# Kernel tuning notes

Hardware: AMD Instinct MI355X
Metric: run time of the kernel (lower is better)

Reference implementation:

```python
import jax, jax.numpy as jnp
import numpy as np

N_BATCH, CH, HW, KERNEL, STRIDE, VC = 8, 256, 96, 8, 3, 512


def setup_inputs() -> dict:
    key = jax.random.key(0)
    k0, k1, k2, k3 = jax.random.split(key, 4)
    kk = KERNEL * KERNEL
    x = jax.random.normal(k0, (N_BATCH, CH, HW, HW), dtype=jnp.float32)
    # 1x1 conv weight [vc, ch, 1, 1] stored as [vc, ch]
    conv_w = jax.random.normal(k1, (VC, CH), dtype=jnp.float32) * 0.05
    # integrate_mask_activation: Linear(ch+kk, 3ch) -> LeakyReLU(0.2) -> Linear(3ch, ch) -> Tanh
    W1 = jax.random.normal(k2, (3 * CH, CH + kk), dtype=jnp.float32) * 0.02
    b1 = jnp.zeros((3 * CH,), dtype=jnp.float32)
    W2 = jax.random.normal(k3, (CH, 3 * CH), dtype=jnp.float32) * 0.02
    b2 = jnp.zeros((CH,), dtype=jnp.float32)
    return {"x": x, "conv_w": conv_w, "W1": W1, "b1": b1, "W2": W2, "b2": b2}


def _unfold(x, k, s):
    # torch.nn.Unfold(kernel=(k,k), stride=s) -> patches [n, L, c, k, k]
    n, c, h, w = x.shape
    oh = (h - k) // s + 1
    ow = (w - k) // s + 1
    ih = (jnp.arange(oh) * s)[:, None] + jnp.arange(k)[None, :]  # [oh, k]
    iw = (jnp.arange(ow) * s)[:, None] + jnp.arange(k)[None, :]  # [ow, k]
    p = x[:, :, ih, :]          # [n, c, oh, k, w]
    p = p[:, :, :, :, iw]       # [n, c, oh, k, ow, k]
    p = p.transpose(0, 2, 4, 1, 3, 5)  # [n, oh, ow, c, k, k]
    return p.reshape(n, oh * ow, c, k, k), oh * ow


def reference(x, conv_w, W1, b1, W2, b2):
    k = KERNEL
    kk = k * k
    n, c, h, w = x.shape
    patches, L = _unfold(x, k, STRIDE)           # [n, L, c, k, k]
    N = n * L
    p = patches.reshape(N, c, k, k)

    # GenerateMask_2_0: normalized similarity via 1x1 conv
    x_norm = jnp.sqrt((p ** 2).sum(1))           # [N, k, k]
    w_norm = jnp.sqrt((conv_w ** 2).sum(1))      # [vc]
    y = jnp.einsum('nchw,vc->nvhw', p, conv_w)   # [N, vc, k, k]
    y = y / (x_norm[:, None, :, :] * w_norm[None, :, None, None])

    vc = conv_w.shape[0]
    y_flat = y.reshape(N, vc * kk)
    idx = jnp.argmax(y_flat, axis=1)                       # topk(k=1)
    max_sim = jnp.take_along_axis(y_flat, idx[:, None], axis=1)  # [N, 1]
    max_ch = idx // kk                                     # codebook index [N]
    col = idx % kk                                         # spatial index [N]

    rows = jnp.arange(N)
    sim_map_max = y.reshape(N, vc, kk)[rows, max_ch]       # [N, kk]
    max_act = p.reshape(N, c, kk)[rows, :, col]            # [N, c]
    vc_vec = conv_w[max_ch]                                # [N, c]
    integ = max_act * max_sim + vc_vec * (1.0 - max_sim)   # blend with codebook

    # integrate_mask_activation MLP
    inp = jnp.concatenate([integ, sim_map_max], axis=1)    # [N, c + kk]
    h1 = inp @ W1.T + b1
    h1 = jnp.where(h1 > 0, h1, 0.2 * h1)                   # LeakyReLU(0.2)
    out = jnp.tanh(h1 @ W2.T + b2)                         # [N, c]
    return out.reshape(n, L, c)
```

## Files before the change

kernel.cpp:

```cpp
#include <hip/hip_runtime.h>
#include <hip/hip_fp16.h>
#include <math.h>

#define NB 8
#define CHN 256
#define HWD 96
#define PIXN (HWD*HWD)
#define TOTPIX (NB*PIXN)
#define VCN 512
#define OHW 30
#define LPP (OHW*OHW)
#define NPATCH (NB*LPP)
#define INPD 320
#define HID 768
#define MTP 456

typedef unsigned short u16;
typedef __attribute__((ext_vector_type(8))) short bf16x8;
typedef __attribute__((ext_vector_type(8))) unsigned short us8;
typedef __attribute__((ext_vector_type(4))) float f32x4;

__device__ __forceinline__ float f4c(const float4 v, int i){
  return i==0 ? v.x : i==1 ? v.y : i==2 ? v.z : v.w;
}
__device__ __forceinline__ u16 bfrn(float f){
  unsigned u = __float_as_uint(f);
  return (u16)((u + 0x7fffu + ((u>>16)&1u)) >> 16);
}
__device__ __forceinline__ float bf2f(u16 h){
  return __uint_as_float(((unsigned)h)<<16);
}


template<int NS>
__device__ __forceinline__ void split_body(const float* __restrict__ src,
                                           u16* __restrict__ dst, int K,
                                           int rt, int kk, int kkc, int lane){
  const int qr = lane>>4, col = lane&15;
  const float* s = src + (size_t)(rt*16+col)*K + kk*32 + qr*8;
  us8 h1, h2, h3;
  #pragma unroll
  for (int j=0;j<8;j++){
    float a = s[j];
    u16 x1 = bfrn(a);  float r1 = a - bf2f(x1);
    u16 x2 = bfrn(r1); float r2 = r1 - bf2f(x2);
    h1[j]=x1; h2[j]=x2; h3[j]=bfrn(r2);
  }
  size_t base = ((size_t)(rt*kkc + kk)*NS)*512 + lane*8;
  *(us8*)&dst[base]     = h1;
  *(us8*)&dst[base+512] = h2;
  if (NS == 3) *(us8*)&dst[base+1024] = h3;
}

__global__ __launch_bounds__(64) void prep_k(
    const float* __restrict__ cw, const float* __restrict__ W1,
    const float* __restrict__ W2, u16* __restrict__ wf,
    u16* __restrict__ w1f, u16* __restrict__ w2f, float* __restrict__ invw){
  int b = blockIdx.x;
  const int lane = threadIdx.x;
  if (b < 256){ split_body<3>(cw, wf, CHN, b>>3, b&7, 8, lane); return; }
  b -= 256;
  if (b < 480){ split_body<2>(W1, w1f, INPD, b/10, b%10, 10, lane); return; }
  b -= 480;
  if (b < 384){ split_body<2>(W2, w2f, HID, b/24, b%24, 24, lane); return; }
  b -= 384;
  const float4 a = *(const float4*)&cw[(size_t)b*CHN + lane*4];
  float s = fmaf(a.x,a.x, fmaf(a.y,a.y, fmaf(a.z,a.z, a.w*a.w)));
  #pragma unroll
  for (int off=32; off; off>>=1) s += __shfl_xor(s, off);
  if (lane==0) invw[b] = 1.0f/sqrtf(s);
}

__device__ __forceinline__ void mfma6(f32x4& c, const bf16x8* A, const bf16x8* B){
  c = __builtin_amdgcn_mfma_f32_16x16x32_bf16(A[0], B[0], c, 0,0,0);
  c = __builtin_amdgcn_mfma_f32_16x16x32_bf16(A[0], B[1], c, 0,0,0);
  c = __builtin_amdgcn_mfma_f32_16x16x32_bf16(A[1], B[0], c, 0,0,0);
  c = __builtin_amdgcn_mfma_f32_16x16x32_bf16(A[0], B[2], c, 0,0,0);
  c = __builtin_amdgcn_mfma_f32_16x16x32_bf16(A[1], B[1], c, 0,0,0);
  c = __builtin_amdgcn_mfma_f32_16x16x32_bf16(A[2], B[0], c, 0,0,0);
}

__global__ __launch_bounds__(256,3) void gemm_z_k(
    const float* __restrict__ x, const u16* __restrict__ wf,
    const float* __restrict__ invw,
    float* __restrict__ pbest, int* __restrict__ pbidx,
    __half* __restrict__ zf){
  __shared__ __align__(16) u16 afr[2*8*3*512];
  __shared__ float ssq2[4][32];
  __shared__ float rv[32][4];
  __shared__ int   ri[32][4];
  const int t = threadIdx.x;
  const int wv = t>>6, lane = t&63;
  const int col = lane&15, qr = lane>>4;
  const size_t p0 = (size_t)blockIdx.x * 32;
  const int img = (int)(p0 / PIXN);
  const int pl0 = (int)(p0 % PIXN);

  {
    const int pi = t & 31, bq = t >> 5;
    const int fr = pi & 15, mt = pi >> 4;
    const float* xb = x + ((size_t)img*CHN)*PIXN + pl0 + pi;
    float s = 0.f;
    #pragma unroll
    for (int it=0; it<4; ++it){
      const int c0 = it*64 + bq*8;
      float xv[8];
      #pragma unroll
      for (int j=0;j<8;j++) xv[j] = xb[(size_t)(c0+j)*PIXN];
      us8 h1,h2,h3;
      #pragma unroll
      for (int j=0;j<8;j++){
        const float a = xv[j];
        s = fmaf(a,a,s);
        u16 x1 = bfrn(a);  float r1 = a - bf2f(x1);
        u16 x2 = bfrn(r1);
        h1[j]=x1; h2[j]=x2; h3[j]=bfrn(r1 - bf2f(x2));
      }
      const int kk = c0 >> 5, cq = (c0>>3)&3;
      u16* dstp = &afr[((mt*8+kk)*3)*512 + (cq*16+fr)*8];
      *(us8*)dstp        = h1;
      *(us8*)(dstp+512)  = h2;
      *(us8*)(dstp+1024) = h3;
    }
    s += __shfl_xor(s, 32);
    if (lane < 32) ssq2[wv][lane] = s;
  }
  __syncthreads();

  f32x4 acc[2][8];
  #pragma unroll
  for (int i=0;i<2;i++)
    #pragma unroll
    for (int j=0;j<8;j++) acc[i][j] = (f32x4){0.f,0.f,0.f,0.f};
  const size_t loff = (size_t)lane*8;
  const int loff16 = lane*8;
  for (int kk=0; kk<8; ++kk){
    bf16x8 a0[3], a1[3];
    {
      const int ab0 = (kk*3)*512 + loff16;
      const int ab1 = ((8+kk)*3)*512 + loff16;
      a0[0] = *(const bf16x8*)&afr[ab0];
      a0[1] = *(const bf16x8*)&afr[ab0+512];
      a0[2] = *(const bf16x8*)&afr[ab0+1024];
      a1[0] = *(const bf16x8*)&afr[ab1];
      a1[1] = *(const bf16x8*)&afr[ab1+512];
      a1[2] = *(const bf16x8*)&afr[ab1+1024];
    }
    #pragma unroll
    for (int h=0; h<2; ++h){
      bf16x8 bg[4][3];
      #pragma unroll
      for (int q=0;q<4;q++){
        const int ni = h*4+q;
        const size_t bb = (((size_t)(wv*8+ni)*8 + kk)*3)*512 + loff;
        bg[q][0] = *(const bf16x8*)&wf[bb];
        bg[q][1] = *(const bf16x8*)&wf[bb+512];
        bg[q][2] = *(const bf16x8*)&wf[bb+1024];
      }
      #pragma unroll
      for (int q=0;q<4;q++){
        const int ni = h*4+q;
        mfma6(acc[0][ni], a0, bg[q]);
        mfma6(acc[1][ni], a1, bg[q]);
      }
    }
  }

  float iw[8];
  #pragma unroll
  for (int ni=0;ni<8;ni++) iw[ni] = invw[wv*128 + ni*16 + col];
  #pragma unroll
  for (int mi=0;mi<2;mi++){
    #pragma unroll
    for (int r=0;r<4;r++){
      const int P2 = mi*16 + qr*4 + r;
      const float sq = ssq2[0][P2] + ssq2[1][P2] + ssq2[2][P2] + ssq2[3][P2];
      const float ip = rsqrtf(sq);
      float bz = -1e30f; int bvi = 0;
      #pragma unroll
      for (int ni=0;ni<8;ni++){
        const float z = f4c(*(const float4*)&acc[mi][ni], r) * ip * iw[ni];
        const int vv = wv*128 + ni*16 + col;
        zf[(p0+P2)*VCN + vv] = __float2half(z);
        if (z > bz){ bz = z; bvi = vv; }
      }
      #pragma unroll
      for (int off=1; off<16; off<<=1){
        const float oz = __shfl_xor(bz, off);
        const int  oi = __shfl_xor(bvi, off);
        if (oz > bz || (oz == bz && oi < bvi)){ bz = oz; bvi = oi; }
      }
      if (col == 0){ rv[P2][wv] = bz; ri[P2][wv] = bvi; }
    }
  }
  __syncthreads();
  if (t < 32){
    float best = rv[t][0]; int bi = ri[t][0];
    #pragma unroll
    for (int s=1;s<4;s++){
      float z2 = rv[t][s]; int i2 = ri[t][s];
      if (z2 > best || (z2 == best && i2 < bi)){ best = z2; bi = i2; }
    }
    pbest[p0+t] = best; pbidx[p0+t] = bi;
  }
}

__global__ __launch_bounds__(64) void select_k(
    const float* __restrict__ x, const float* __restrict__ cw,
    const __half* __restrict__ zf,
    const float* __restrict__ pbest, const int* __restrict__ pbidx,
    u16* __restrict__ inpf){
  __shared__ float wlds[256];
  __shared__ float xcol[256];
  __shared__ float simv[64];
  const int q = blockIdx.x;
  const int lane = threadIdx.x;
  const int n = q / LPP, l = q % LPP;
  const int oy = l / OHW, ox = l % OHW;
  const int pl = (oy*3 + (lane >> 3))*HWD + (ox*3 + (lane & 7));
  const int p = n*PIXN + pl;
  const int rt = q >> 4, ql = q & 15;
  float val = pbest[p];
  int flat = pbidx[p]*64 + lane;
  #pragma unroll
  for (int off=32; off>0; off>>=1){
    float ov = __shfl_xor(val, off);
    int of = __shfl_xor(flat, off);
    if (ov > val || (ov == val && of < flat)){ val = ov; flat = of; }
  }
  const int mch = flat >> 6;
  const int pos = flat & 63;
  const float ms = val;
  *(float4*)&wlds[lane*4] = *(const float4*)&cw[(size_t)mch*CHN + lane*4];
  simv[lane] = __half2float(zf[(size_t)p*VCN + mch]);
  const int wpl = (oy*3 + (pos>>3))*HWD + (ox*3 + (pos&7));
  const float* xb = x + (size_t)n*CHN*PIXN + wpl;
  #pragma unroll
  for (int j=0;j<4;j++) xcol[lane*4+j] = xb[(size_t)(lane*4+j)*PIXN];
  __syncthreads();
  if (lane < 32){
    const int kk = lane >> 2, qr = lane & 3;
    const float om = 1.0f - ms;
    const int c0 = kk*32 + qr*8;
    us8 p1, p2;
    #pragma unroll
    for (int j=0;j<8;j++){
      float v = fmaf(xcol[c0+j], ms, wlds[c0+j]*om);
      u16 s1 = bfrn(v);
      p1[j] = s1; p2[j] = bfrn(v - bf2f(s1));
    }
    const size_t ob = ((size_t)(rt*10 + kk)*2)*512 + (qr*16 + ql)*8;
    *(us8*)&inpf[ob]     = p1;
    *(us8*)&inpf[ob+512] = p2;
  }
  if (lane < 16){
    const int s = lane >> 3, kk = 8 + ((lane >> 2) & 1), qr = lane & 3;
    us8 pv;
    #pragma unroll
    for (int j=0;j<8;j++){
      float v = simv[(kk-8)*32 + qr*8 + j];
      u16 s1 = bfrn(v);
      pv[j] = (s == 0) ? s1 : bfrn(v - bf2f(s1));
    }
    const size_t ob = ((size_t)(rt*10 + kk)*2 + s)*512 + (qr*16 + ql)*8;
    *(us8*)&inpf[ob] = pv;
  }
}

__global__ __launch_bounds__(256,2) void mlp1_k(
    const u16* __restrict__ af, const u16* __restrict__ bf,
    const float* __restrict__ bias, u16* __restrict__ h1f){
  const int kkc = INPD >> 5;
  const int t = threadIdx.x;
  const int n0 = blockIdx.x*128, m0 = blockIdx.y*128;
  const int lane = t&63, wv = t>>6;
  const int mq = wv&1, nq = wv>>1;
  const int col = lane&15, qr = lane>>4;
  const size_t loff = (size_t)lane*8;
  const int ptA0 = (m0>>4) + mq*4;
  const int ntB0 = (n0>>4) + nq*4;
  f32x4 acc[4][4];
  #pragma unroll
  for (int i=0;i<4;i++)
    #pragma unroll
    for (int j=0;j<4;j++) acc[i][j] = (f32x4){0.f,0.f,0.f,0.f};

  for (int kk=0; kk<kkc; kk++){
    bf16x8 a[4][2];
    #pragma unroll
    for (int mi=0;mi<4;mi++){
      const size_t ab = (((size_t)(ptA0+mi)*kkc + kk)*2)*512 + loff;
      a[mi][0] = *(const bf16x8*)&af[ab];
      a[mi][1] = *(const bf16x8*)&af[ab+512];
    }
    #pragma unroll
    for (int ni=0;ni<4;ni++){
      const size_t bb = (((size_t)(ntB0+ni)*kkc + kk)*2)*512 + loff;
      const bf16x8 b1 = *(const bf16x8*)&bf[bb];
      const bf16x8 b2 = *(const bf16x8*)&bf[bb+512];
      #pragma unroll
      for (int mi=0;mi<4;mi++){
        f32x4 c = acc[mi][ni];
        c = __builtin_amdgcn_mfma_f32_16x16x32_bf16(a[mi][0], b1, c, 0,0,0);
        c = __builtin_amdgcn_mfma_f32_16x16x32_bf16(a[mi][0], b2, c, 0,0,0);
        c = __builtin_amdgcn_mfma_f32_16x16x32_bf16(a[mi][1], b1, c, 0,0,0);
        acc[mi][ni] = c;
      }
    }
  }
  float bb4[4];
  #pragma unroll
  for (int ni=0;ni<4;ni++) bb4[ni] = bias[n0 + nq*64 + ni*16 + col];
  #pragma unroll
  for (int mi=0;mi<4;mi++){
    const int rt2 = (m0>>4) + mq*4 + mi;
    #pragma unroll
    for (int r=0;r<4;r++){
      #pragma unroll
      for (int ni=0;ni<4;ni++){
        float v = f4c(*(const float4*)&acc[mi][ni], r) + bb4[ni];
        v = v > 0.f ? v : 0.2f*v;
        u16 s1 = bfrn(v);
        u16 s2 = bfrn(v - bf2f(s1));
        const int kk2 = (n0>>5) + nq*2 + (ni>>1);
        const int qn = (ni&1)*2 + (col>>3);
        const size_t ob = ((size_t)(rt2*24 + kk2)*2)*512 + (qn*16 + qr*4 + r)*8 + (col&7);
        h1f[ob] = s1; h1f[ob+512] = s2;
      }
    }
  }
}

__global__ __launch_bounds__(256,2) void mlp2_k(
    const u16* __restrict__ af, const u16* __restrict__ bf,
    const float* __restrict__ bias, float* __restrict__ C){
  const int kkc = HID >> 5;
  const int t = threadIdx.x;
  const int n0 = blockIdx.x*128, m0 = blockIdx.y*128;
  const int lane = t&63, wv = t>>6;
  const int mq = wv&1, nq = wv>>1;
  const int col = lane&15, qr = lane>>4;
  const size_t loff = (size_t)lane*8;
  const int ptA0 = (m0>>4) + mq*4;
  const int ntB0 = (n0>>4) + nq*4;
  f32x4 acc[4][4];
  #pragma unroll
  for (int i=0;i<4;i++)
    #pragma unroll
    for (int j=0;j<4;j++) acc[i][j] = (f32x4){0.f,0.f,0.f,0.f};

  for (int kk=0; kk<kkc; kk++){
    bf16x8 a[4][2];
    #pragma unroll
    for (int mi=0;mi<4;mi++){
      const size_t ab = (((size_t)(ptA0+mi)*kkc + kk)*2)*512 + loff;
      a[mi][0] = *(const bf16x8*)&af[ab];
      a[mi][1] = *(const bf16x8*)&af[ab+512];
    }
    #pragma unroll
    for (int ni=0;ni<4;ni++){
      const size_t bb = (((size_t)(ntB0+ni)*kkc + kk)*2)*512 + loff;
      const bf16x8 b1 = *(const bf16x8*)&bf[bb];
      const bf16x8 b2 = *(const bf16x8*)&bf[bb+512];
      #pragma unroll
      for (int mi=0;mi<4;mi++){
        f32x4 c = acc[mi][ni];
        c = __builtin_amdgcn_mfma_f32_16x16x32_bf16(a[mi][0], b1, c, 0,0,0);
        c = __builtin_amdgcn_mfma_f32_16x16x32_bf16(a[mi][0], b2, c, 0,0,0);
        c = __builtin_amdgcn_mfma_f32_16x16x32_bf16(a[mi][1], b1, c, 0,0,0);
        acc[mi][ni] = c;
      }
    }
  }
  float bb4[4];
  #pragma unroll
  for (int ni=0;ni<4;ni++) bb4[ni] = bias[n0 + nq*64 + ni*16 + col];
  #pragma unroll
  for (int mi=0;mi<4;mi++){
    #pragma unroll
    for (int r=0;r<4;r++){
      const int row = m0 + mq*64 + mi*16 + qr*4 + r;
      if (row < NPATCH){
        #pragma unroll
        for (int ni=0;ni<4;ni++){
          float v = f4c(*(const float4*)&acc[mi][ni], r) + bb4[ni];
          C[(size_t)row*CHN + n0 + nq*64 + ni*16 + col] = tanhf(v);
        }
      }
    }
  }
}

extern "C" void kernel_launch(void* const* d_in, const int* in_sizes, int n_in,
                              void* d_out, int out_size, void* d_ws, size_t ws_size,
                              hipStream_t stream){
  const float* x  = (const float*)d_in[0];
  const float* cw = (const float*)d_in[1];
  const float* W1 = (const float*)d_in[2];
  const float* b1 = (const float*)d_in[3];
  const float* W2 = (const float*)d_in[4];
  const float* b2 = (const float*)d_in[5];
  float* out = (float*)d_out;
  float* ws = (float*)d_ws;
  float* invw  = ws;
  float* pbest = invw + VCN;
  int*   pbidx = (int*)(pbest + TOTPIX);
  u16*   wf    = (u16*)(pbidx + TOTPIX);
  u16*   w1f   = wf + (size_t)32*8*3*512;
  u16*   w2f   = w1f + (size_t)48*10*2*512;
  u16*   inpf  = w2f + (size_t)16*24*2*512;
  __half* zf   = (__half*)(inpf + (size_t)MTP*10*2*512);
  u16*   h1f   = (u16*)zf;

  prep_k<<<1632,64,0,stream>>>(cw, W1, W2, wf, w1f, w2f, invw);
  gemm_z_k<<<TOTPIX/32,256,0,stream>>>(x, wf, invw, pbest, pbidx, zf);
  select_k<<<NPATCH,64,0,stream>>>(x, cw, zf, pbest, pbidx, inpf);
  mlp1_k<<<dim3(HID/128, (NPATCH+127)/128),256,0,stream>>>(inpf, w1f, b1, h1f);
  mlp2_k<<<dim3(CHN/128, (NPATCH+127)/128),256,0,stream>>>(h1f, w2f, b2, out);
}
```

Before: 326.4 us.

## Fuse all stages into one persistent kernel with grid-wide barriers

Replaces the five separate launches (weight prep, similarity GEMM, patch selection, two MLP GEMMs) with one persistent kernel. Its grid is sized from the occupancy query and it loops over the work units of each stage, separated by atomic-counter grid barriers. The aim is to remove launch gaps and tail effects between stages. In exchange it uses spin barriers that depend on every block being co-resident, and the MLP stages now run at a different occupancy than their original launch bounds. The old multi-kernel path remains as a fallback.

```diff
diff --git a/kernel.cpp b/kernel.cpp
--- a/kernel.cpp
+++ b/kernel.cpp
@@ -52,25 +52,6 @@
   if (NS == 3) *(us8*)&dst[base+1024] = h3;
 }
 
-__global__ __launch_bounds__(64) void prep_k(
-    const float* __restrict__ cw, const float* __restrict__ W1,
-    const float* __restrict__ W2, u16* __restrict__ wf,
-    u16* __restrict__ w1f, u16* __restrict__ w2f, float* __restrict__ invw){
-  int b = blockIdx.x;
-  const int lane = threadIdx.x;
-  if (b < 256){ split_body<3>(cw, wf, CHN, b>>3, b&7, 8, lane); return; }
-  b -= 256;
-  if (b < 480){ split_body<2>(W1, w1f, INPD, b/10, b%10, 10, lane); return; }
-  b -= 480;
-  if (b < 384){ split_body<2>(W2, w2f, HID, b/24, b%24, 24, lane); return; }
-  b -= 384;
-  const float4 a = *(const float4*)&cw[(size_t)b*CHN + lane*4];
-  float s = fmaf(a.x,a.x, fmaf(a.y,a.y, fmaf(a.z,a.z, a.w*a.w)));
-  #pragma unroll
-  for (int off=32; off; off>>=1) s += __shfl_xor(s, off);
-  if (lane==0) invw[b] = 1.0f/sqrtf(s);
-}
-
 __device__ __forceinline__ void mfma6(f32x4& c, const bf16x8* A, const bf16x8* B){
   c = __builtin_amdgcn_mfma_f32_16x16x32_bf16(A[0], B[0], c, 0,0,0);
   c = __builtin_amdgcn_mfma_f32_16x16x32_bf16(A[0], B[1], c, 0,0,0);
@@ -80,19 +61,36 @@
   c = __builtin_amdgcn_mfma_f32_16x16x32_bf16(A[2], B[0], c, 0,0,0);
 }
 
-__global__ __launch_bounds__(256,3) void gemm_z_k(
+
+__device__ __forceinline__ void prep_unit(int u, int lane,
+    const float* __restrict__ cw, const float* __restrict__ W1,
+    const float* __restrict__ W2, u16* __restrict__ wf,
+    u16* __restrict__ w1f, u16* __restrict__ w2f, float* __restrict__ invw){
+  if (u < 256){ split_body<3>(cw, wf, CHN, u>>3, u&7, 8, lane); return; }
+  u -= 256;
+  if (u < 480){ split_body<2>(W1, w1f, INPD, u/10, u%10, 10, lane); return; }
+  u -= 480;
+  if (u < 384){ split_body<2>(W2, w2f, HID, u/24, u%24, 24, lane); return; }
+  u -= 384;
+  const float4 a = *(const float4*)&cw[(size_t)u*CHN + lane*4];
+  float s = fmaf(a.x,a.x, fmaf(a.y,a.y, fmaf(a.z,a.z, a.w*a.w)));
+  #pragma unroll
+  for (int off=32; off; off>>=1) s += __shfl_xor(s, off);
+  if (lane==0) invw[u] = 1.0f/sqrtf(s);
+}
+
+__device__ __forceinline__ void gemm_tile(int tile, int t, unsigned char* smem,
     const float* __restrict__ x, const u16* __restrict__ wf,
     const float* __restrict__ invw,
     float* __restrict__ pbest, int* __restrict__ pbidx,
     __half* __restrict__ zf){
-  __shared__ __align__(16) u16 afr[2*8*3*512];
-  __shared__ float ssq2[4][32];
-  __shared__ float rv[32][4];
-  __shared__ int   ri[32][4];
-  const int t = threadIdx.x;
+  u16* afr          = (u16*)smem;
+  float (*ssq2)[32] = (float(*)[32])(smem + 49152);
+  float (*rv)[4]    = (float(*)[4]) (smem + 49152 + 512);
+  int   (*ri)[4]    = (int(*)[4])  (smem + 49152 + 1024);
   const int wv = t>>6, lane = t&63;
   const int col = lane&15, qr = lane>>4;
-  const size_t p0 = (size_t)blockIdx.x * 32;
+  const size_t p0 = (size_t)tile * 32;
   const int img = (int)(p0 / PIXN);
   const int pl0 = (int)(p0 % PIXN);
 
@@ -203,76 +201,79 @@
     }
     pbest[p0+t] = best; pbidx[p0+t] = bi;
   }
-}
-
-__global__ __launch_bounds__(64) void select_k(
+  __syncthreads();
+}
+
+struct SelWS { float wlds[256]; float xcol[256]; float simv[64]; };
+
+__device__ __forceinline__ void select_patch(int q, bool act, int lane, SelWS* sw,
     const float* __restrict__ x, const float* __restrict__ cw,
     const __half* __restrict__ zf,
     const float* __restrict__ pbest, const int* __restrict__ pbidx,
     u16* __restrict__ inpf){
-  __shared__ float wlds[256];
-  __shared__ float xcol[256];
-  __shared__ float simv[64];
-  const int q = blockIdx.x;
-  const int lane = threadIdx.x;
-  const int n = q / LPP, l = q % LPP;
-  const int oy = l / OHW, ox = l % OHW;
-  const int pl = (oy*3 + (lane >> 3))*HWD + (ox*3 + (lane & 7));
-  const int p = n*PIXN + pl;
-  const int rt = q >> 4, ql = q & 15;
-  float val = pbest[p];
-  int flat = pbidx[p]*64 + lane;
-  #pragma unroll
-  for (int off=32; off>0; off>>=1){
-    float ov = __shfl_xor(val, off);
-    int of = __shfl_xor(flat, off);
-    if (ov > val || (ov == val && of < flat)){ val = ov; flat = of; }
-  }
-  const int mch = flat >> 6;
-  const int pos = flat & 63;
-  const float ms = val;
-  *(float4*)&wlds[lane*4] = *(const float4*)&cw[(size_t)mch*CHN + lane*4];
-  simv[lane] = __half2float(zf[(size_t)p*VCN + mch]);
-  const int wpl = (oy*3 + (pos>>3))*HWD + (ox*3 + (pos&7));
-  const float* xb = x + (size_t)n*CHN*PIXN + wpl;
-  #pragma unroll
-  for (int j=0;j<4;j++) xcol[lane*4+j] = xb[(size_t)(lane*4+j)*PIXN];
-  __syncthreads();
-  if (lane < 32){
-    const int kk = lane >> 2, qr = lane & 3;
-    const float om = 1.0f - ms;
-    const int c0 = kk*32 + qr*8;
-    us8 p1, p2;
-    #pragma unroll
-    for (int j=0;j<8;j++){
-      float v = fmaf(xcol[c0+j], ms, wlds[c0+j]*om);
-      u16 s1 = bfrn(v);
-      p1[j] = s1; p2[j] = bfrn(v - bf2f(s1));
-    }
-    const size_t ob = ((size_t)(rt*10 + kk)*2)*512 + (qr*16 + ql)*8;
-    *(us8*)&inpf[ob]     = p1;
-    *(us8*)&inpf[ob+512] = p2;
-  }
-  if (lane < 16){
-    const int s = lane >> 3, kk = 8 + ((lane >> 2) & 1), qr = lane & 3;
-    us8 pv;
-    #pragma unroll
-    for (int j=0;j<8;j++){
-      float v = simv[(kk-8)*32 + qr*8 + j];
-      u16 s1 = bfrn(v);
-      pv[j] = (s == 0) ? s1 : bfrn(v - bf2f(s1));
-    }
-    const size_t ob = ((size_t)(rt*10 + kk)*2 + s)*512 + (qr*16 + ql)*8;
-    *(us8*)&inpf[ob] = pv;
-  }
-}
-
-__global__ __launch_bounds__(256,2) void mlp1_k(
+  float ms = 0.f; int pos = 0;
+  int rt = 0, ql = 0;
+  if (act){
+    const int l = q % LPP; const int n = q / LPP;
+    const int oy = l / OHW, ox = l % OHW;
+    const int pl = (oy*3 + (lane >> 3))*HWD + (ox*3 + (lane & 7));
+    const int p = n*PIXN + pl;
+    rt = q >> 4; ql = q & 15;
+    float val = pbest[p];
+    int flat = pbidx[p]*64 + lane;
+    #pragma unroll
+    for (int off=32; off>0; off>>=1){
+      float ov = __shfl_xor(val, off);
+      int of = __shfl_xor(flat, off);
+      if (ov > val || (ov == val && of < flat)){ val = ov; flat = of; }
+    }
+    const int mch = flat >> 6;
+    pos = flat & 63;
+    ms = val;
+    *(float4*)&sw->wlds[lane*4] = *(const float4*)&cw[(size_t)mch*CHN + lane*4];
+    sw->simv[lane] = __half2float(zf[(size_t)p*VCN + mch]);
+    const int wpl = (oy*3 + (pos>>3))*HWD + (ox*3 + (pos&7));
+    const float* xw = x + (size_t)n*CHN*PIXN + wpl;
+    #pragma unroll
+    for (int j=0;j<4;j++) sw->xcol[lane*4+j] = xw[(size_t)(lane*4+j)*PIXN];
+  }
+  __syncthreads();
+  if (act){
+    if (lane < 32){
+      const int kk = lane >> 2, qrr = lane & 3;
+      const float om = 1.0f - ms;
+      const int c0 = kk*32 + qrr*8;
+      us8 p1, p2;
+      #pragma unroll
+      for (int j=0;j<8;j++){
+        float v = fmaf(sw->xcol[c0+j], ms, sw->wlds[c0+j]*om);
+        u16 s1 = bfrn(v);
+        p1[j] = s1; p2[j] = bfrn(v - bf2f(s1));
+      }
+      const size_t ob = ((size_t)(rt*10 + kk)*2)*512 + (qrr*16 + ql)*8;
+      *(us8*)&inpf[ob]     = p1;
+      *(us8*)&inpf[ob+512] = p2;
+    }
+    if (lane < 16){
+      const int s = lane >> 3, kk = 8 + ((lane >> 2) & 1), qrr = lane & 3;
+      us8 pv;
+      #pragma unroll
+      for (int j=0;j<8;j++){
+        float v = sw->simv[(kk-8)*32 + qrr*8 + j];
+        u16 s1 = bfrn(v);
+        pv[j] = (s == 0) ? s1 : bfrn(v - bf2f(s1));
+      }
+      const size_t ob = ((size_t)(rt*10 + kk)*2 + s)*512 + (qrr*16 + ql)*8;
+      *(us8*)&inpf[ob] = pv;
+    }
+  }
+  __syncthreads();
+}
+
+__device__ __forceinline__ void mlp1_body(int n0, int m0, int t,
     const u16* __restrict__ af, const u16* __restrict__ bf,
     const float* __restrict__ bias, u16* __restrict__ h1f){
   const int kkc = INPD >> 5;
-  const int t = threadIdx.x;
-  const int n0 = blockIdx.x*128, m0 = blockIdx.y*128;
   const int lane = t&63, wv = t>>6;
   const int mq = wv&1, nq = wv>>1;
   const int col = lane&15, qr = lane>>4;
@@ -284,7 +285,6 @@
   for (int i=0;i<4;i++)
     #pragma unroll
     for (int j=0;j<4;j++) acc[i][j] = (f32x4){0.f,0.f,0.f,0.f};
-
   for (int kk=0; kk<kkc; kk++){
     bf16x8 a[4][2];
     #pragma unroll
@@ -331,12 +331,10 @@
   }
 }
 
-__global__ __launch_bounds__(256,2) void mlp2_k(
+__device__ __forceinline__ void mlp2_body(int n0, int m0, int t,
     const u16* __restrict__ af, const u16* __restrict__ bf,
     const float* __restrict__ bias, float* __restrict__ C){
   const int kkc = HID >> 5;
-  const int t = threadIdx.x;
-  const int n0 = blockIdx.x*128, m0 = blockIdx.y*128;
   const int lane = t&63, wv = t>>6;
   const int mq = wv&1, nq = wv>>1;
   const int col = lane&15, qr = lane>>4;
@@ -348,7 +346,6 @@
   for (int i=0;i<4;i++)
     #pragma unroll
     for (int j=0;j<4;j++) acc[i][j] = (f32x4){0.f,0.f,0.f,0.f};
-
   for (int kk=0; kk<kkc; kk++){
     bf16x8 a[4][2];
     #pragma unroll
@@ -389,6 +386,94 @@
       }
     }
   }
+}
+
+__device__ __forceinline__ void gbar(int* ctr, int nblk){
+  __syncthreads();
+  if (threadIdx.x == 0){
+    __threadfence();
+    atomicAdd(ctr, 1);
+    while (__hip_atomic_load(ctr, __ATOMIC_RELAXED, __HIP_MEMORY_SCOPE_AGENT) < nblk)
+      __builtin_amdgcn_s_sleep(8);
+    __threadfence();
+  }
+  __syncthreads();
+}
+
+__global__ __launch_bounds__(256,3) void mega_k(
+    const float* __restrict__ x, const float* __restrict__ cw,
+    const float* __restrict__ W1, const float* __restrict__ b1,
+    const float* __restrict__ W2, const float* __restrict__ b2,
+    u16* __restrict__ wf, u16* __restrict__ w1f, u16* __restrict__ w2f,
+    float* __restrict__ invw,
+    float* __restrict__ pbest, int* __restrict__ pbidx,
+    __half* __restrict__ zf, u16* __restrict__ inpf, u16* __restrict__ h1f,
+    float* __restrict__ out, int* __restrict__ bar){
+  __shared__ __align__(16) unsigned char smem[50688];
+  const int t = threadIdx.x;
+  const int wv = t>>6, lane = t&63;
+  const int nblk = (int)gridDim.x;
+
+  for (int u = blockIdx.x*4 + wv; u < 1632; u += nblk*4)
+    prep_unit(u, lane, cw, W1, W2, wf, w1f, w2f, invw);
+  gbar(bar+0, nblk);
+
+  for (int tile = blockIdx.x; tile < TOTPIX/32; tile += nblk)
+    gemm_tile(tile, t, smem, x, wf, invw, pbest, pbidx, zf);
+  gbar(bar+1, nblk);
+
+  {
+    SelWS* sws = (SelWS*)smem;
+    for (int base = 0; base < NPATCH; base += nblk*4){
+      const int q = base + blockIdx.x*4 + wv;
+      select_patch(q, q < NPATCH, lane, &sws[wv], x, cw, zf, pbest, pbidx, inpf);
+    }
+  }
+  gbar(bar+2, nblk);
+
+  for (int vb = blockIdx.x; vb < 6*57; vb += nblk)
+    mlp1_body((vb%6)*128, (vb/6)*128, t, inpf, w1f, b1, h1f);
+  gbar(bar+3, nblk);
+
+  for (int vb = blockIdx.x; vb < 2*57; vb += nblk)
+    mlp2_body((vb%2)*128, (vb/2)*128, t, h1f, w2f, b2, out);
+}
+
+__global__ __launch_bounds__(64) void prep_k(
+    const float* __restrict__ cw, const float* __restrict__ W1,
+    const float* __restrict__ W2, u16* __restrict__ wf,
+    u16* __restrict__ w1f, u16* __restrict__ w2f, float* __restrict__ invw){
+  prep_unit(blockIdx.x, threadIdx.x, cw, W1, W2, wf, w1f, w2f, invw);
+}
+
+__global__ __launch_bounds__(256,3) void gemm_z_k(
+    const float* __restrict__ x, const u16* __restrict__ wf,
+    const float* __restrict__ invw,
+    float* __restrict__ pbest, int* __restrict__ pbidx,
+    __half* __restrict__ zf){
+  __shared__ __align__(16) unsigned char smem[50688];
+  gemm_tile(blockIdx.x, threadIdx.x, smem, x, wf, invw, pbest, pbidx, zf);
+}
+
+__global__ __launch_bounds__(64) void select_k(
+    const float* __restrict__ x, const float* __restrict__ cw,
+    const __half* __restrict__ zf,
+    const float* __restrict__ pbest, const int* __restrict__ pbidx,
+    u16* __restrict__ inpf){
+  __shared__ SelWS sw;
+  select_patch(blockIdx.x, true, threadIdx.x, &sw, x, cw, zf, pbest, pbidx, inpf);
+}
+
+__global__ __launch_bounds__(256,2) void mlp1_k(
+    const u16* __restrict__ af, const u16* __restrict__ bf,
+    const float* __restrict__ bias, u16* __restrict__ h1f){
+  mlp1_body(blockIdx.x*128, blockIdx.y*128, threadIdx.x, af, bf, bias, h1f);
+}
+
+__global__ __launch_bounds__(256,2) void mlp2_k(
+    const u16* __restrict__ af, const u16* __restrict__ bf,
+    const float* __restrict__ bias, float* __restrict__ C){
+  mlp2_body(blockIdx.x*128, blockIdx.y*128, threadIdx.x, af, bf, bias, C);
 }
 
 extern "C" void kernel_launch(void* const* d_in, const int* in_sizes, int n_in,
@@ -402,7 +487,8 @@
   const float* b2 = (const float*)d_in[5];
   float* out = (float*)d_out;
   float* ws = (float*)d_ws;
-  float* invw  = ws;
+  int*   bar   = (int*)ws;
+  float* invw  = ws + 8;
   float* pbest = invw + VCN;
   int*   pbidx = (int*)(pbest + TOTPIX);
   u16*   wf    = (u16*)(pbidx + TOTPIX);
@@ -412,9 +498,18 @@
   __half* zf   = (__half*)(inpf + (size_t)MTP*10*2*512);
   u16*   h1f   = (u16*)zf;
 
-  prep_k<<<1632,64,0,stream>>>(cw, W1, W2, wf, w1f, w2f, invw);
-  gemm_z_k<<<TOTPIX/32,256,0,stream>>>(x, wf, invw, pbest, pbidx, zf);
-  select_k<<<NPATCH,64,0,stream>>>(x, cw, zf, pbest, pbidx, inpf);
-  mlp1_k<<<dim3(HID/128, (NPATCH+127)/128),256,0,stream>>>(inpf, w1f, b1, h1f);
-  mlp2_k<<<dim3(CHN/128, (NPATCH+127)/128),256,0,stream>>>(h1f, w2f, b2, out);
-}
+  int nb = 0;
+  hipError_t qe = hipOccupancyMaxActiveBlocksPerMultiprocessor(&nb, mega_k, 256, 0);
+  if (qe == hipSuccess && nb >= 2){
+    const int grid = (nb >= 3 ? 3 : 2) * 256;
+    hipMemsetAsync(bar, 0, 8*sizeof(int), stream);
+    mega_k<<<grid,256,0,stream>>>(x, cw, W1, b1, W2, b2, wf, w1f, w2f, invw,
+                                  pbest, pbidx, zf, inpf, h1f, out, bar);
+  } else {
+    prep_k<<<1632,64,0,stream>>>(cw, W1, W2, wf, w1f, w2f, invw);
+    gemm_z_k<<<TOTPIX/32,256,0,stream>>>(x, wf, invw, pbest, pbidx, zf);
+    select_k<<<NPATCH,64,0,stream>>>(x, cw, zf, pbest, pbidx, inpf);
+    mlp1_k<<<dim3(HID/128, (NPATCH+127)/128),256,0,stream>>>(inpf, w1f, b1, h1f);
+    mlp2_k<<<dim3(CHN/128, (NPATCH+127)/128),256,0,stream>>>(h1f, w2f, b2, out);
+  }
+}
```

New measurement: 326.7 us. Within noise of the previous version (+0.1%).

## Enlarge GEMM pixel tile to 64 with 8 waves and two-phase K staging

Applied to the files above, without the earlier changes.

The similarity GEMM kernel now processes 64 pixels per block with 512 threads (8 waves), each wave covering 64 codebook vectors across 4 M-tiles instead of 128 vectors across 2. This halves the codebook weight fetches per pixel. The K dimension is staged through LDS in two halves to keep shared memory bounded, with a skew added between M-tiles to reduce bank conflicts. The cost is an extra barrier, occupancy limited to one block per CU via launch bounds, and higher register pressure from the 4x4 accumulators.

```diff
diff --git a/kernel.cpp b/kernel.cpp
--- a/kernel.cpp
+++ b/kernel.cpp
@@ -80,29 +80,43 @@
   c = __builtin_amdgcn_mfma_f32_16x16x32_bf16(A[2], B[0], c, 0,0,0);
 }
 
-__global__ __launch_bounds__(256,3) void gemm_z_k(
+#define AFR_MT_STRIDE (4*3*512)
+#define AFR_SKEW 32
+__global__ __launch_bounds__(512,1) void gemm_z_k(
     const float* __restrict__ x, const u16* __restrict__ wf,
     const float* __restrict__ invw,
     float* __restrict__ pbest, int* __restrict__ pbidx,
     __half* __restrict__ zf){
-  __shared__ __align__(16) u16 afr[2*8*3*512];
-  __shared__ float ssq2[4][32];
-  __shared__ float rv[32][4];
-  __shared__ int   ri[32][4];
+  __shared__ __align__(16) u16 afr[4*AFR_MT_STRIDE + 4*AFR_SKEW];
+  __shared__ float ssq8[8][64];
+  __shared__ float rv[64][8];
+  __shared__ int   ri[64][8];
   const int t = threadIdx.x;
   const int wv = t>>6, lane = t&63;
   const int col = lane&15, qr = lane>>4;
-  const size_t p0 = (size_t)blockIdx.x * 32;
+  const size_t p0 = (size_t)blockIdx.x * 64;
   const int img = (int)(p0 / PIXN);
   const int pl0 = (int)(p0 % PIXN);
 
-  {
-    const int pi = t & 31, bq = t >> 5;
-    const int fr = pi & 15, mt = pi >> 4;
-    const float* xb = x + ((size_t)img*CHN)*PIXN + pl0 + pi;
-    float s = 0.f;
-    #pragma unroll
-    for (int it=0; it<4; ++it){
+  const int pi = t & 63, bq = t >> 6;
+  const int fr = pi & 15, mt = pi >> 4;
+  const float* xb = x + ((size_t)img*CHN)*PIXN + pl0 + pi;
+  float ssum = 0.f;
+
+  f32x4 acc[4][4];
+  #pragma unroll
+  for (int i=0;i<4;i++)
+    #pragma unroll
+    for (int j=0;j<4;j++) acc[i][j] = (f32x4){0.f,0.f,0.f,0.f};
+  const size_t loff = (size_t)lane*8;
+  const int loff16 = lane*8;
+  const int vt0 = wv*4;
+
+  #pragma unroll 1
+  for (int ph=0; ph<2; ++ph){
+    #pragma unroll
+    for (int il=0; il<2; ++il){
+      const int it = ph*2 + il;
       const int c0 = it*64 + bq*8;
       float xv[8];
       #pragma unroll
@@ -111,76 +125,67 @@
       #pragma unroll
       for (int j=0;j<8;j++){
         const float a = xv[j];
-        s = fmaf(a,a,s);
+        ssum = fmaf(a,a,ssum);
         u16 x1 = bfrn(a);  float r1 = a - bf2f(x1);
         u16 x2 = bfrn(r1);
         h1[j]=x1; h2[j]=x2; h3[j]=bfrn(r1 - bf2f(x2));
       }
-      const int kk = c0 >> 5, cq = (c0>>3)&3;
-      u16* dstp = &afr[((mt*8+kk)*3)*512 + (cq*16+fr)*8];
+      const int kkl = (c0 >> 5) - ph*4, cq = (c0>>3)&3;
+      u16* dstp = &afr[mt*AFR_MT_STRIDE + mt*AFR_SKEW + kkl*1536 + (cq*16+fr)*8];
       *(us8*)dstp        = h1;
       *(us8*)(dstp+512)  = h2;
       *(us8*)(dstp+1024) = h3;
     }
-    s += __shfl_xor(s, 32);
-    if (lane < 32) ssq2[wv][lane] = s;
-  }
-  __syncthreads();
-
-  f32x4 acc[2][8];
-  #pragma unroll
-  for (int i=0;i<2;i++)
-    #pragma unroll
-    for (int j=0;j<8;j++) acc[i][j] = (f32x4){0.f,0.f,0.f,0.f};
-  const size_t loff = (size_t)lane*8;
-  const int loff16 = lane*8;
-  for (int kk=0; kk<8; ++kk){
-    bf16x8 a0[3], a1[3];
-    {
-      const int ab0 = (kk*3)*512 + loff16;
-      const int ab1 = ((8+kk)*3)*512 + loff16;
-      a0[0] = *(const bf16x8*)&afr[ab0];
-      a0[1] = *(const bf16x8*)&afr[ab0+512];
-      a0[2] = *(const bf16x8*)&afr[ab0+1024];
-      a1[0] = *(const bf16x8*)&afr[ab1];
-      a1[1] = *(const bf16x8*)&afr[ab1+512];
-      a1[2] = *(const bf16x8*)&afr[ab1+1024];
-    }
-    #pragma unroll
-    for (int h=0; h<2; ++h){
+    if (ph == 1) ssq8[bq][pi] = ssum;
+    __syncthreads();
+
+    #pragma unroll 1
+    for (int kk=0; kk<4; ++kk){
+      const int kkg = ph*4 + kk;
+      bf16x8 a[4][3];
+      #pragma unroll
+      for (int mi=0;mi<4;mi++){
+        const int ab = mi*AFR_MT_STRIDE + mi*AFR_SKEW + kk*1536 + loff16;
+        a[mi][0] = *(const bf16x8*)&afr[ab];
+        a[mi][1] = *(const bf16x8*)&afr[ab+512];
+        a[mi][2] = *(const bf16x8*)&afr[ab+1024];
+      }
       bf16x8 bg[4][3];
       #pragma unroll
       for (int q=0;q<4;q++){
-        const int ni = h*4+q;
-        const size_t bb = (((size_t)(wv*8+ni)*8 + kk)*3)*512 + loff;
+        const size_t bb = (((size_t)(vt0+q)*8 + kkg)*3)*512 + loff;
         bg[q][0] = *(const bf16x8*)&wf[bb];
         bg[q][1] = *(const bf16x8*)&wf[bb+512];
         bg[q][2] = *(const bf16x8*)&wf[bb+1024];
       }
       #pragma unroll
-      for (int q=0;q<4;q++){
-        const int ni = h*4+q;
-        mfma6(acc[0][ni], a0, bg[q]);
-        mfma6(acc[1][ni], a1, bg[q]);
-      }
-    }
-  }
-
-  float iw[8];
-  #pragma unroll
-  for (int ni=0;ni<8;ni++) iw[ni] = invw[wv*128 + ni*16 + col];
-  #pragma unroll
-  for (int mi=0;mi<2;mi++){
+      for (int q=0;q<4;q++)
+        #pragma unroll
+        for (int mi=0;mi<4;mi++)
+          mfma6(acc[mi][q], a[mi], bg[q]);
+    }
+    if (ph == 0) __syncthreads();
+  }
+
+  float iw[4];
+  #pragma unroll
+  for (int ni=0;ni<4;ni++) iw[ni] = invw[wv*64 + ni*16 + col];
+  #pragma unroll
+  for (int mi=0;mi<4;mi++){
     #pragma unroll
     for (int r=0;r<4;r++){
       const int P2 = mi*16 + qr*4 + r;
-      const float sq = ssq2[0][P2] + ssq2[1][P2] + ssq2[2][P2] + ssq2[3][P2];
+      const float t01 = ssq8[0][P2] + ssq8[1][P2];
+      const float t23 = ssq8[2][P2] + ssq8[3][P2];
+      const float t45 = ssq8[4][P2] + ssq8[5][P2];
+      const float t67 = ssq8[6][P2] + ssq8[7][P2];
+      const float sq = ((t01 + t23) + t45) + t67;
       const float ip = rsqrtf(sq);
       float bz = -1e30f; int bvi = 0;
       #pragma unroll
-      for (int ni=0;ni<8;ni++){
+      for (int ni=0;ni<4;ni++){
         const float z = f4c(*(const float4*)&acc[mi][ni], r) * ip * iw[ni];
-        const int vv = wv*128 + ni*16 + col;
+        const int vv = wv*64 + ni*16 + col;
         zf[(p0+P2)*VCN + vv] = __float2half(z);
         if (z > bz){ bz = z; bvi = vv; }
       }
@@ -194,10 +199,10 @@
     }
   }
   __syncthreads();
-  if (t < 32){
+  if (t < 64){
     float best = rv[t][0]; int bi = ri[t][0];
     #pragma unroll
-    for (int s=1;s<4;s++){
+    for (int s=1;s<8;s++){
       float z2 = rv[t][s]; int i2 = ri[t][s];
       if (z2 > best || (z2 == best && i2 < bi)){ best = z2; bi = i2; }
     }
@@ -413,7 +418,7 @@
   u16*   h1f   = (u16*)zf;
 
   prep_k<<<1632,64,0,stream>>>(cw, W1, W2, wf, w1f, w2f, invw);
-  gemm_z_k<<<TOTPIX/32,256,0,stream>>>(x, wf, invw, pbest, pbidx, zf);
+  gemm_z_k<<<TOTPIX/64,512,0,stream>>>(x, wf, invw, pbest, pbidx, zf);
   select_k<<<NPATCH,64,0,stream>>>(x, cw, zf, pbest, pbidx, inpf);
   mlp1_k<<<dim3(HID/128, (NPATCH+127)/128),256,0,stream>>>(inpf, w1f, b1, h1f);
   mlp2_k<<<dim3(CHN/128, (NPATCH+127)/128),256,0,stream>>>(h1f, w2f, b2, out);
```

Result: slower. 356.7 us (+9.3%).
